# Performance work log

Hardware: AMD Instinct MI355X
Metric: run time of the kernel (lower is better)

## Reference

```python
import jax, jax.numpy as jnp
import numpy as np

B, D_IN, D_F = 4096, 1024, 256   # batch, extractor input dim, feature dim
M, K = 10, 8                      # n_mixtures, n_components per mixture
LOG2PI = float(np.log(2.0 * np.pi))


def setup_inputs() -> dict:
    key = jax.random.key(0)
    k0, k1, k2, k3, k4 = jax.random.split(key, 5)
    x = jax.random.normal(k0, (B, D_IN), jnp.float32)
    W = jax.random.normal(k1, (D_IN, D_F), jnp.float32) / np.sqrt(D_IN)
    b = jnp.zeros((D_F,), jnp.float32)
    means = jax.random.normal(k2, (M, K, D_F), jnp.float32)
    # full covariance parameter; tril is taken in forward; +I keeps the
    # Cholesky-factor diagonal positive, as torch MultivariateNormal requires
    covs = jax.random.normal(k3, (M, K, D_F, D_F), jnp.float32) * 0.01
    covs = covs + jnp.eye(D_F, dtype=jnp.float32)
    weights = jax.random.normal(k4, (M, K), jnp.float32)
    return {"x": x, "W": W, "b": b, "means": means, "covs": covs, "weights": weights}


def reference(x, W, b, means, covs, weights):
    # extractor: Linear + ReLU -> [B, D_F]
    feats = jax.nn.relu(x @ W + b)
    # scale_tril = tril(cov) for every (mixture, component): [M, K, D_F, D_F]
    L = jnp.tril(covs)
    # diff between every feature vector and every component mean: [M, K, B, D_F]
    diff = feats[None, None, :, :] - means[:, :, None, :]
    # batched triangular solve L z = diff^T -> z: [M, K, D_F, B]
    z = jax.scipy.linalg.solve_triangular(L, jnp.swapaxes(diff, -1, -2), lower=True)
    quad = jnp.sum(z * z, axis=-2)  # Mahalanobis term: [M, K, B]
    logdet = jnp.sum(jnp.log(jnp.diagonal(L, axis1=-2, axis2=-1)), axis=-1)  # [M, K]
    logp = -0.5 * (quad + D_F * LOG2PI) - logdet[..., None]  # MVN log_prob: [M, K, B]
    # per-mixture softmax over component weights, multiply into log-probs
    w = jax.nn.softmax(weights, axis=-1)  # [M, K]
    mix = w[..., None] * logp             # [M, K, B]
    # GMM returns [B, K]; DeepGMM stacks over mixtures and transposes -> [B, M, K]
    return jnp.transpose(mix, (2, 0, 1))
```

## Files before the change

### kernel.cpp

```cpp
#include <hip/hip_runtime.h>

#define B_N 4096
#define D_IN 1024
#define D_F 256
#define MK 80
#define LOG2PI 1.8378770664093453f
#define XP_S 72

typedef float f32x4 __attribute__((ext_vector_type(4)));
typedef short bf16x8 __attribute__((ext_vector_type(8)));
typedef float float4_ __attribute__((ext_vector_type(4)));
typedef unsigned int u32x4 __attribute__((ext_vector_type(4)));
typedef unsigned short u16x8 __attribute__((ext_vector_type(8)));

__device__ __forceinline__ unsigned short f2bf(float f) {
    unsigned u = __float_as_uint(f);
    u += 0x7fffu + ((u >> 16) & 1u);
    return (unsigned short)(u >> 16);
}
__device__ __forceinline__ float bf2f(unsigned short h) {
    return __uint_as_float(((unsigned)h) << 16);
}
__device__ __forceinline__ void gload_lds16(const void* g, void* l) {
    __builtin_amdgcn_global_load_lds((const __attribute__((address_space(1))) void*)g,
                                     (__attribute__((address_space(3))) void*)l, 16, 0, 0);
}
__device__ __forceinline__ bf16x8 pack8(float4_ a, float4_ b) {
    bf16x8 r;
    r[0] = (short)f2bf(a.x); r[1] = (short)f2bf(a.y);
    r[2] = (short)f2bf(a.z); r[3] = (short)f2bf(a.w);
    r[4] = (short)f2bf(b.x); r[5] = (short)f2bf(b.y);
    r[6] = (short)f2bf(b.z); r[7] = (short)f2bf(b.w);
    return r;
}

__global__ __launch_bounds__(256) void k_pre(const float* __restrict__ W,
                                             const float* __restrict__ covs,
                                             const float* __restrict__ wts,
                                             unsigned short* __restrict__ wt,
                                             float* __restrict__ wmix,
                                             float* __restrict__ ldet,
                                             unsigned short* __restrict__ covsb) {
    int bx = blockIdx.x, tid = threadIdx.x;
    if (bx < 64) {
        __shared__ unsigned short t[64][65];
        int k0 = (bx >> 2) * 64, n0 = (bx & 3) * 64;
        int r = tid / 64, c = tid % 64;
        #pragma unroll
        for (int rr = r; rr < 64; rr += 4)
            t[rr][c] = f2bf(W[(size_t)(k0 + rr) * D_F + n0 + c]);
        __syncthreads();
        #pragma unroll
        for (int rr = r; rr < 64; rr += 4)
            wt[(size_t)(n0 + rr) * D_IN + k0 + c] = t[c][rr];
    } else if (bx < 144) {
        if (tid < 64) {
            int mk = bx - 64;
            int l = tid;
            const float* Lm = covs + (size_t)mk * D_F * D_F;
            float s = 0.0f;
            for (int i = l; i < D_F; i += 64) s += logf(Lm[(size_t)i * D_F + i]);
            for (int off = 32; off; off >>= 1) s += __shfl_down(s, off);
            if (l == 0) {
                ldet[mk] = s;
                int m = mk / 8, k = mk % 8;
                float mx = -1e30f;
                for (int j = 0; j < 8; j++) mx = fmaxf(mx, wts[m * 8 + j]);
                float sum = 0.0f;
                for (int j = 0; j < 8; j++) sum += expf(wts[m * 8 + j] - mx);
                wmix[mk] = expf(wts[m * 8 + k] - mx) / sum;
            }
        }
    } else if (bx < 224) {
        int mk = bx - 144;
        const float* Cm = covs + (size_t)mk * D_F * D_F;
        unsigned short* Cb = covsb + (size_t)mk * 10 * 4096;
        #pragma unroll
        for (int I = 1; I < 4; ++I)
            for (int K = 0; K < I; ++K) {
                int idx = (I * (I - 1)) / 2 + K;
                for (int t4 = tid; t4 < 1024; t4 += 256) {
                    int r = t4 >> 4, kq = t4 & 15;
                    float4_ v = *(const float4_*)&Cm[(size_t)(I * 64 + r) * D_F
                                                     + K * 64 + kq * 4];
                    ushort4 o;
                    o.x = f2bf(v.x); o.y = f2bf(v.y); o.z = f2bf(v.z); o.w = f2bf(v.w);
                    *(ushort4*)&Cb[(size_t)idx * 4096 + r * 64 + kq * 4] = o;
                }
            }
    } else {
        int b = bx - 224;
        int mk = b >> 2, I = b & 3;
        int i0 = I * 64;
        __shared__ float rl[64];
        __shared__ unsigned short X[64][XP_S];
        __shared__ unsigned short Yt[2][64][XP_S];
        int w = tid >> 6, l = tid & 63;
        const float* Cm = covs + (size_t)mk * D_F * D_F;
        if (tid < 64) rl[tid] = 1.0f / Cm[(size_t)(i0 + tid) * D_F + i0 + tid];
        __syncthreads();
        for (int t4 = tid; t4 < 1024; t4 += 256) {
            int r = t4 >> 4, kq = t4 & 15;
            float4_ v = *(const float4_*)&Cm[(size_t)(i0 + r) * D_F + i0 + kq * 4];
            float ri = rl[r];
            int base = kq * 4;
            ushort4 o;
            o.x = (base     < r) ? f2bf(v.x * ri) : (unsigned short)0;
            o.y = (base + 1 < r) ? f2bf(v.y * ri) : (unsigned short)0;
            o.z = (base + 2 < r) ? f2bf(v.z * ri) : (unsigned short)0;
            o.w = (base + 3 < r) ? f2bf(v.w * ri) : (unsigned short)0;
            *(ushort4*)&X[r][base] = o;
        }
        __syncthreads();
        for (int t = tid; t < 4096; t += 256) {
            int j = t >> 6, i = t & 63;
            unsigned short xv = X[i][j];
            Yt[0][j][i] = (i == j) ? (unsigned short)0x3F80
                                   : (unsigned short)(xv ^ 0x8000u);
        }
        __syncthreads();
        int cur = 0;
        for (int it = 0; it < 3; ++it) {
            bf16x8 a0 = *(const bf16x8*)&Yt[cur][16 * w + (l & 15)][(l >> 4) * 8];
            bf16x8 a1 = *(const bf16x8*)&Yt[cur][16 * w + (l & 15)][32 + (l >> 4) * 8];
            f32x4 acc[4] = {{0, 0, 0, 0}, {0, 0, 0, 0}, {0, 0, 0, 0}, {0, 0, 0, 0}};
            #pragma unroll
            for (int ni = 0; ni < 4; ++ni) {
                bf16x8 b0 = *(const bf16x8*)&X[ni * 16 + (l & 15)][(l >> 4) * 8];
                bf16x8 b1 = *(const bf16x8*)&X[ni * 16 + (l & 15)][32 + (l >> 4) * 8];
                acc[ni] = __builtin_amdgcn_mfma_f32_16x16x32_bf16(a0, b0, acc[ni], 0, 0, 0);
                acc[ni] = __builtin_amdgcn_mfma_f32_16x16x32_bf16(a1, b1, acc[ni], 0, 0, 0);
            }
            #pragma unroll
            for (int ni = 0; ni < 4; ++ni)
                #pragma unroll
                for (int q = 0; q < 4; ++q) {
                    int i = ni * 16 + (l & 15);
                    int j = 16 * w + (l >> 4) * 4 + q;
                    float v = ((i == j) ? 1.0f : 0.0f) - acc[ni][q];
                    Yt[cur ^ 1][j][i] = f2bf(v);
                }
            __syncthreads();
            cur ^= 1;
        }
        unsigned short* Xg = covsb + ((size_t)mk * 10 + 6 + I) * 4096;
        for (int t = tid; t < 4096; t += 256) {
            int r = t >> 6, c = t & 63;
            Xg[t] = f2bf(bf2f(Yt[cur][c][r]) * rl[c]);
        }
    }
}

__global__ __launch_bounds__(256) void k_inv_panel(
        const unsigned short* __restrict__ covsb,
        const float* __restrict__ means,
        unsigned short* __restrict__ linv,
        float* __restrict__ cpart) {
    int mk = blockIdx.x, J = blockIdx.y;
    int jc0 = J * 64;
    __shared__ unsigned short Xp[4][64][XP_S];
    __shared__ unsigned short Sb[64][XP_S];
    __shared__ float muS[64];
    int tid = threadIdx.x, w = tid >> 6, l = tid & 63;
    const unsigned short* Cb = covsb + (size_t)mk * 10 * 4096;
    const unsigned short* Dmk = Cb + 6 * 4096;
    unsigned short* Lout = linv + (size_t)mk * D_F * D_F;

    for (int t = tid; t < jc0 * 8; t += 256) {
        int r = t >> 3, s = t & 7;
        ((u32x4*)(Lout + (size_t)r * D_F + jc0))[s] = (u32x4){0, 0, 0, 0};
    }
    const unsigned short* DJ = Dmk + J * 4096;
    for (int t = tid; t < 4096; t += 256) {
        int r = t >> 6, c = t & 63;
        Xp[J][c][r] = DJ[t];
    }
    for (int t = tid; t < 512; t += 256) {
        int r = t >> 3, s = t & 7;
        ((u32x4*)(Lout + (size_t)(jc0 + r) * D_F + jc0))[s] = ((const u32x4*)(DJ + r * 64))[s];
    }
    __syncthreads();

    for (int I = J + 1; I < 4; ++I) {
        f32x4 acc[4] = {};
        for (int K = J; K < I; ++K) {
            const unsigned short* CB = Cb + (size_t)((I * (I - 1)) / 2 + K) * 4096;
            #pragma unroll
            for (int kb = 0; kb < 2; ++kb) {
                bf16x8 af = *(const bf16x8*)&Xp[K][w * 16 + (l & 15)][kb * 32 + (l >> 4) * 8];
                #pragma unroll
                for (int ni = 0; ni < 4; ++ni) {
                    bf16x8 bf = *(const bf16x8*)&CB[(size_t)(ni * 16 + (l & 15)) * 64
                                                    + kb * 32 + (l >> 4) * 8];
                    acc[ni] = __builtin_amdgcn_mfma_f32_16x16x32_bf16(af, bf, acc[ni], 0, 0, 0);
                }
            }
        }
        #pragma unroll
        for (int ni = 0; ni < 4; ++ni)
            #pragma unroll
            for (int q = 0; q < 4; ++q)
                Sb[w * 16 + ((l >> 4) << 2) + q][ni * 16 + (l & 15)] = f2bf(acc[ni][q]);
        __syncthreads();
        f32x4 acc2[4] = {};
        #pragma unroll
        for (int kb = 0; kb < 2; ++kb) {
            bf16x8 af = *(const bf16x8*)&Sb[w * 16 + (l & 15)][kb * 32 + (l >> 4) * 8];
            #pragma unroll
            for (int ni = 0; ni < 4; ++ni) {
                const u16x8* dp = (const u16x8*)(Dmk + (size_t)I * 4096
                                  + (ni * 16 + (l & 15)) * 64 + kb * 32 + (l >> 4) * 8);
                u16x8 dv = *dp ^ (unsigned short)0x8000;
                bf16x8 bf = __builtin_bit_cast(bf16x8, dv);
                acc2[ni] = __builtin_amdgcn_mfma_f32_16x16x32_bf16(af, bf, acc2[ni], 0, 0, 0);
            }
        }
        #pragma unroll
        for (int ni = 0; ni < 4; ++ni)
            #pragma unroll
            for (int q = 0; q < 4; ++q) {
                int c = w * 16 + ((l >> 4) << 2) + q;
                int r = ni * 16 + (l & 15);
                unsigned short hv = f2bf(acc2[ni][q]);
                Xp[I][c][r] = hv;
                Lout[(size_t)(I * 64 + r) * D_F + jc0 + c] = hv;
            }
        __syncthreads();
    }

    if (tid < 64) muS[tid] = means[(size_t)mk * D_F + jc0 + tid];
    __syncthreads();
    {
        int I = w, r = l;
        float s = 0.0f;
        if (I >= J) {
            for (int c = 0; c < 64; ++c)
                s += bf2f(Xp[I][c][r]) * muS[c];
        }
        cpart[((size_t)mk * 4 + J) * 256 + tid] = s;
    }
}

__global__ __launch_bounds__(256) void k_feat(const float* __restrict__ x,
                                              const unsigned short* __restrict__ wt,
                                              const float* __restrict__ bias,
                                              unsigned short* __restrict__ fb) {
    __shared__ unsigned short As[64][128];
    __shared__ unsigned short Bs[64][128];
    int b0 = blockIdx.x * 64;
    int n0 = blockIdx.y * 64;
    int tid = threadIdx.x, w = tid >> 6, l = tid & 63;
    int wm = w >> 1, wn = w & 1;
    f32x4 acc[2][2] = {};
    for (int k0 = 0; k0 < D_IN; k0 += 128) {
        float4_ av[4][2];
        #pragma unroll
        for (int it = 0; it < 4; ++it) {
            int o16 = tid + it * 256;
            int r = o16 >> 4, c = o16 & 15;
            const float* gp = x + (size_t)(b0 + r) * D_IN + k0 + c * 8;
            av[it][0] = *(const float4_*)gp;
            av[it][1] = *(const float4_*)(gp + 4);
        }
        __syncthreads();
        #pragma unroll
        for (int it = 0; it < 4; ++it) {
            int o16 = tid + it * 256;
            int r = o16 >> 4, c = o16 & 15;
            int cs = c ^ (r & 7);
            *(bf16x8*)&As[r][cs * 8] = pack8(av[it][0], av[it][1]);
            gload_lds16(wt + (size_t)(n0 + r) * D_IN + k0 + cs * 8, &Bs[0][0] + o16 * 8);
        }
        __syncthreads();
        #pragma unroll
        for (int ks = 0; ks < 4; ++ks) {
            int uw = ((ks * 4 + (l >> 4)) ^ (l & 7)) * 8;
            bf16x8 af[2], bg[2];
            #pragma unroll
            for (int mi = 0; mi < 2; ++mi)
                af[mi] = *(const bf16x8*)&As[wm * 32 + mi * 16 + (l & 15)][uw];
            #pragma unroll
            for (int ni = 0; ni < 2; ++ni)
                bg[ni] = *(const bf16x8*)&Bs[wn * 32 + ni * 16 + (l & 15)][uw];
            #pragma unroll
            for (int mi = 0; mi < 2; ++mi)
                #pragma unroll
                for (int ni = 0; ni < 2; ++ni)
                    acc[mi][ni] = __builtin_amdgcn_mfma_f32_16x16x32_bf16(
                        af[mi], bg[ni], acc[mi][ni], 0, 0, 0);
        }
    }
    #pragma unroll
    for (int mi = 0; mi < 2; ++mi)
        #pragma unroll
        for (int ni = 0; ni < 2; ++ni) {
            int d = n0 + wn * 32 + ni * 16 + (l & 15);
            float bia = bias[d];
            #pragma unroll
            for (int r = 0; r < 4; ++r) {
                int b = b0 + wm * 32 + mi * 16 + (l >> 4) * 4 + r;
                float v = fmaxf(acc[mi][ni][r] + bia, 0.0f);
                fb[(size_t)b * D_F + d] = f2bf(v);
            }
        }
}

__global__ __launch_bounds__(512) void k_gmm(const unsigned short* __restrict__ linv,
                                             const unsigned short* __restrict__ fb,
                                             const float* __restrict__ cpart,
                                             const float* __restrict__ wmix,
                                             const float* __restrict__ ldet,
                                             float* __restrict__ out) {
    __shared__ unsigned short As[256][64];
    __shared__ unsigned short Bs[128][64];
    __shared__ float cb[D_F];
    __shared__ float qpart[4][128];
    int mk = blockIdx.x;
    int b0 = blockIdx.y * 128;
    int tid = threadIdx.x, w = tid >> 6, l = tid & 63;
    int wm = w >> 1, wn = w & 1;
    const unsigned short* Ab = linv + (size_t)mk * D_F * D_F;
    if (tid < D_F) {
        const float* cp = cpart + (size_t)mk * 4 * D_F + tid;
        cb[tid] = cp[0] + cp[256] + cp[512] + cp[768];
    }
    f32x4 acc[4][4] = {};
    for (int k0 = 0; k0 < D_F; k0 += 64) {
        #pragma unroll
        for (int it = 0; it < 4; ++it) {
            int o16 = tid + it * 512;
            int r = o16 >> 3, c8 = (o16 & 7) ^ (r & 7);
            gload_lds16(Ab + (size_t)r * D_F + k0 + c8 * 8, &As[0][0] + o16 * 8);
        }
        #pragma unroll
        for (int it = 0; it < 2; ++it) {
            int o16 = tid + it * 512;
            int r = o16 >> 3, c8 = (o16 & 7) ^ (r & 7);
            gload_lds16(fb + (size_t)(b0 + r) * D_F + k0 + c8 * 8, &Bs[0][0] + o16 * 8);
        }
        __syncthreads();
        #pragma unroll
        for (int ks = 0; ks < 2; ++ks) {
            int uw = ((ks * 4 + (l >> 4)) ^ (l & 7)) * 8;
            bf16x8 af[4], bg[4];
            #pragma unroll
            for (int mi = 0; mi < 4; ++mi)
                af[mi] = *(const bf16x8*)&As[wm * 64 + mi * 16 + (l & 15)][uw];
            #pragma unroll
            for (int ni = 0; ni < 4; ++ni)
                bg[ni] = *(const bf16x8*)&Bs[wn * 64 + ni * 16 + (l & 15)][uw];
            #pragma unroll
            for (int mi = 0; mi < 4; ++mi)
                #pragma unroll
                for (int ni = 0; ni < 4; ++ni)
                    acc[mi][ni] = __builtin_amdgcn_mfma_f32_16x16x32_bf16(
                        af[mi], bg[ni], acc[mi][ni], 0, 0, 0);
        }
        __syncthreads();
    }
    float p[4] = {0, 0, 0, 0};
    #pragma unroll
    for (int mi = 0; mi < 4; ++mi) {
        int ibase = wm * 64 + mi * 16 + ((l >> 4) << 2);
        #pragma unroll
        for (int r = 0; r < 4; ++r) {
            float cv = cb[ibase + r];
            #pragma unroll
            for (int ni = 0; ni < 4; ++ni) {
                float z = acc[mi][ni][r] - cv;
                p[ni] += z * z;
            }
        }
    }
    #pragma unroll
    for (int ni = 0; ni < 4; ++ni) {
        p[ni] += __shfl_xor(p[ni], 16);
        p[ni] += __shfl_xor(p[ni], 32);
    }
    if (l < 16) {
        #pragma unroll
        for (int ni = 0; ni < 4; ++ni)
            qpart[wm][wn * 64 + ni * 16 + l] = p[ni];
    }
    __syncthreads();
    if (tid < 128) {
        float q = qpart[0][tid] + qpart[1][tid] + qpart[2][tid] + qpart[3][tid];
        float lp = -0.5f * (q + (float)D_F * LOG2PI) - ldet[mk];
        out[(size_t)(b0 + tid) * MK + mk] = wmix[mk] * lp;
    }
}

extern "C" void kernel_launch(void* const* d_in, const int* in_sizes, int n_in,
                              void* d_out, int out_size, void* d_ws, size_t ws_size,
                              hipStream_t stream) {
    const float* x     = (const float*)d_in[0];
    const float* W     = (const float*)d_in[1];
    const float* bias  = (const float*)d_in[2];
    const float* means = (const float*)d_in[3];
    const float* covs  = (const float*)d_in[4];
    const float* wts   = (const float*)d_in[5];
    float* out = (float*)d_out;

    char* ws = (char*)d_ws;
    unsigned short* covsb = (unsigned short*)(ws);
    unsigned short* wt    = (unsigned short*)(ws + 6553600);
    unsigned short* fb    = (unsigned short*)(ws + 7077888);
    unsigned short* linv  = (unsigned short*)(ws + 9175040);
    float* wmix = (float*)(ws + 19742720);
    float* ldet = (float*)(ws + 19743040);
    float* cpart = (float*)(ws + 6553600);

    k_pre<<<dim3(544), dim3(256), 0, stream>>>(W, covs, wts, wt, wmix, ldet, covsb);
    k_feat<<<dim3(64, 4), dim3(256), 0, stream>>>(x, wt, bias, fb);
    k_inv_panel<<<dim3(MK, 4), dim3(256), 0, stream>>>(covsb, means, linv, cpart);
    k_gmm<<<dim3(MK, 32), dim3(512), 0, stream>>>(linv, fb, cpart, wmix, ldet, out);
}
```

Baseline: 82.90 us.

## Merge feature GEMM into preprocessing kernel, split W transpose into own launch

Moves the W transpose into a small standalone kernel and folds the feature GEMM into the former preprocessing kernel as extra blocks, so the GEMM runs alongside the log-det, covariance bf16 conversion and diagonal-block inverse work. Shared memory becomes one 32 KB buffer reused by each branch. The aim is to overlap independent stages and fill the GPU better instead of running them back to back. In exchange, every block of the merged kernel now reserves 32 KB of LDS, which can lower occupancy for the lighter branches.

```diff
diff --git a/kernel.cpp b/kernel.cpp
--- a/kernel.cpp
+++ b/kernel.cpp
@@ -34,28 +34,95 @@
     return r;
 }
 
-__global__ __launch_bounds__(256) void k_pre(const float* __restrict__ W,
+__global__ __launch_bounds__(256) void k_wt(const float* __restrict__ W,
+                                            unsigned short* __restrict__ wt) {
+    __shared__ unsigned short t[64][65];
+    int bx = blockIdx.x, tid = threadIdx.x;
+    int k0 = (bx >> 2) * 64, n0 = (bx & 3) * 64;
+    int r = tid / 64, c = tid % 64;
+    #pragma unroll
+    for (int rr = r; rr < 64; rr += 4)
+        t[rr][c] = f2bf(W[(size_t)(k0 + rr) * D_F + n0 + c]);
+    __syncthreads();
+    #pragma unroll
+    for (int rr = r; rr < 64; rr += 4)
+        wt[(size_t)(n0 + rr) * D_IN + k0 + c] = t[c][rr];
+}
+
+__global__ __launch_bounds__(256) void k_mid(const float* __restrict__ x,
+                                             const unsigned short* __restrict__ wt,
+                                             const float* __restrict__ bias,
                                              const float* __restrict__ covs,
                                              const float* __restrict__ wts,
-                                             unsigned short* __restrict__ wt,
+                                             unsigned short* __restrict__ fb,
                                              float* __restrict__ wmix,
                                              float* __restrict__ ldet,
                                              unsigned short* __restrict__ covsb) {
+    __shared__ char smem[32768];
     int bx = blockIdx.x, tid = threadIdx.x;
-    if (bx < 64) {
-        __shared__ unsigned short t[64][65];
-        int k0 = (bx >> 2) * 64, n0 = (bx & 3) * 64;
-        int r = tid / 64, c = tid % 64;
-        #pragma unroll
-        for (int rr = r; rr < 64; rr += 4)
-            t[rr][c] = f2bf(W[(size_t)(k0 + rr) * D_F + n0 + c]);
-        __syncthreads();
-        #pragma unroll
-        for (int rr = r; rr < 64; rr += 4)
-            wt[(size_t)(n0 + rr) * D_IN + k0 + c] = t[c][rr];
-    } else if (bx < 144) {
+    if (bx < 256) {
+        unsigned short(*As)[128] = (unsigned short(*)[128])smem;
+        unsigned short(*Bs)[128] = (unsigned short(*)[128])(smem + 16384);
+        int b0 = (bx >> 2) * 64;
+        int n0 = (bx & 3) * 64;
+        int w = tid >> 6, l = tid & 63;
+        int wm = w >> 1, wn = w & 1;
+        f32x4 acc[2][2] = {};
+        for (int k0 = 0; k0 < D_IN; k0 += 128) {
+            float4_ av[4][2];
+            #pragma unroll
+            for (int it = 0; it < 4; ++it) {
+                int o16 = tid + it * 256;
+                int r = o16 >> 4, c = o16 & 15;
+                const float* gp = x + (size_t)(b0 + r) * D_IN + k0 + c * 8;
+                av[it][0] = *(const float4_*)gp;
+                av[it][1] = *(const float4_*)(gp + 4);
+            }
+            __syncthreads();
+            #pragma unroll
+            for (int it = 0; it < 4; ++it) {
+                int o16 = tid + it * 256;
+                int r = o16 >> 4, c = o16 & 15;
+                int cs = c ^ (r & 7);
+                *(bf16x8*)&As[r][cs * 8] = pack8(av[it][0], av[it][1]);
+                gload_lds16(wt + (size_t)(n0 + r) * D_IN + k0 + cs * 8,
+                            &Bs[0][0] + o16 * 8);
+            }
+            __syncthreads();
+            #pragma unroll
+            for (int ks = 0; ks < 4; ++ks) {
+                int uw = ((ks * 4 + (l >> 4)) ^ (l & 7)) * 8;
+                bf16x8 af[2], bg[2];
+                #pragma unroll
+                for (int mi = 0; mi < 2; ++mi)
+                    af[mi] = *(const bf16x8*)&As[wm * 32 + mi * 16 + (l & 15)][uw];
+                #pragma unroll
+                for (int ni = 0; ni < 2; ++ni)
+                    bg[ni] = *(const bf16x8*)&Bs[wn * 32 + ni * 16 + (l & 15)][uw];
+                #pragma unroll
+                for (int mi = 0; mi < 2; ++mi)
+                    #pragma unroll
+                    for (int ni = 0; ni < 2; ++ni)
+                        acc[mi][ni] = __builtin_amdgcn_mfma_f32_16x16x32_bf16(
+                            af[mi], bg[ni], acc[mi][ni], 0, 0, 0);
+            }
+        }
+        #pragma unroll
+        for (int mi = 0; mi < 2; ++mi)
+            #pragma unroll
+            for (int ni = 0; ni < 2; ++ni) {
+                int d = n0 + wn * 32 + ni * 16 + (l & 15);
+                float bia = bias[d];
+                #pragma unroll
+                for (int r = 0; r < 4; ++r) {
+                    int b = b0 + wm * 32 + mi * 16 + (l >> 4) * 4 + r;
+                    float v = fmaxf(acc[mi][ni][r] + bia, 0.0f);
+                    fb[(size_t)b * D_F + d] = f2bf(v);
+                }
+            }
+    } else if (bx < 336) {
         if (tid < 64) {
-            int mk = bx - 64;
+            int mk = bx - 256;
             int l = tid;
             const float* Lm = covs + (size_t)mk * D_F * D_F;
             float s = 0.0f;
@@ -71,8 +138,8 @@
                 wmix[mk] = expf(wts[m * 8 + k] - mx) / sum;
             }
         }
-    } else if (bx < 224) {
-        int mk = bx - 144;
+    } else if (bx < 416) {
+        int mk = bx - 336;
         const float* Cm = covs + (size_t)mk * D_F * D_F;
         unsigned short* Cb = covsb + (size_t)mk * 10 * 4096;
         #pragma unroll
@@ -89,12 +156,12 @@
                 }
             }
     } else {
-        int b = bx - 224;
+        int b = bx - 416;
         int mk = b >> 2, I = b & 3;
         int i0 = I * 64;
-        __shared__ float rl[64];
-        __shared__ unsigned short X[64][XP_S];
-        __shared__ unsigned short Yt[2][64][XP_S];
+        float* rl = (float*)smem;
+        unsigned short(*X)[XP_S] = (unsigned short(*)[XP_S])(smem + 256);
+        unsigned short(*Yt)[64][XP_S] = (unsigned short(*)[64][XP_S])(smem + 9472);
         int w = tid >> 6, l = tid & 63;
         const float* Cm = covs + (size_t)mk * D_F * D_F;
         if (tid < 64) rl[tid] = 1.0f / Cm[(size_t)(i0 + tid) * D_F + i0 + tid];
@@ -239,70 +306,6 @@
         }
         cpart[((size_t)mk * 4 + J) * 256 + tid] = s;
     }
-}
-
-__global__ __launch_bounds__(256) void k_feat(const float* __restrict__ x,
-                                              const unsigned short* __restrict__ wt,
-                                              const float* __restrict__ bias,
-                                              unsigned short* __restrict__ fb) {
-    __shared__ unsigned short As[64][128];
-    __shared__ unsigned short Bs[64][128];
-    int b0 = blockIdx.x * 64;
-    int n0 = blockIdx.y * 64;
-    int tid = threadIdx.x, w = tid >> 6, l = tid & 63;
-    int wm = w >> 1, wn = w & 1;
-    f32x4 acc[2][2] = {};
-    for (int k0 = 0; k0 < D_IN; k0 += 128) {
-        float4_ av[4][2];
-        #pragma unroll
-        for (int it = 0; it < 4; ++it) {
-            int o16 = tid + it * 256;
-            int r = o16 >> 4, c = o16 & 15;
-            const float* gp = x + (size_t)(b0 + r) * D_IN + k0 + c * 8;
-            av[it][0] = *(const float4_*)gp;
-            av[it][1] = *(const float4_*)(gp + 4);
-        }
-        __syncthreads();
-        #pragma unroll
-        for (int it = 0; it < 4; ++it) {
-            int o16 = tid + it * 256;
-            int r = o16 >> 4, c = o16 & 15;
-            int cs = c ^ (r & 7);
-            *(bf16x8*)&As[r][cs * 8] = pack8(av[it][0], av[it][1]);
-            gload_lds16(wt + (size_t)(n0 + r) * D_IN + k0 + cs * 8, &Bs[0][0] + o16 * 8);
-        }
-        __syncthreads();
-        #pragma unroll
-        for (int ks = 0; ks < 4; ++ks) {
-            int uw = ((ks * 4 + (l >> 4)) ^ (l & 7)) * 8;
-            bf16x8 af[2], bg[2];
-            #pragma unroll
-            for (int mi = 0; mi < 2; ++mi)
-                af[mi] = *(const bf16x8*)&As[wm * 32 + mi * 16 + (l & 15)][uw];
-            #pragma unroll
-            for (int ni = 0; ni < 2; ++ni)
-                bg[ni] = *(const bf16x8*)&Bs[wn * 32 + ni * 16 + (l & 15)][uw];
-            #pragma unroll
-            for (int mi = 0; mi < 2; ++mi)
-                #pragma unroll
-                for (int ni = 0; ni < 2; ++ni)
-                    acc[mi][ni] = __builtin_amdgcn_mfma_f32_16x16x32_bf16(
-                        af[mi], bg[ni], acc[mi][ni], 0, 0, 0);
-        }
-    }
-    #pragma unroll
-    for (int mi = 0; mi < 2; ++mi)
-        #pragma unroll
-        for (int ni = 0; ni < 2; ++ni) {
-            int d = n0 + wn * 32 + ni * 16 + (l & 15);
-            float bia = bias[d];
-            #pragma unroll
-            for (int r = 0; r < 4; ++r) {
-                int b = b0 + wm * 32 + mi * 16 + (l >> 4) * 4 + r;
-                float v = fmaxf(acc[mi][ni][r] + bia, 0.0f);
-                fb[(size_t)b * D_F + d] = f2bf(v);
-            }
-        }
 }
 
 __global__ __launch_bounds__(512) void k_gmm(const unsigned short* __restrict__ linv,
@@ -410,8 +413,9 @@
     float* ldet = (float*)(ws + 19743040);
     float* cpart = (float*)(ws + 6553600);
 
-    k_pre<<<dim3(544), dim3(256), 0, stream>>>(W, covs, wts, wt, wmix, ldet, covsb);
-    k_feat<<<dim3(64, 4), dim3(256), 0, stream>>>(x, wt, bias, fb);
+    k_wt<<<dim3(64), dim3(256), 0, stream>>>(W, wt);
+    k_mid<<<dim3(736), dim3(256), 0, stream>>>(x, wt, bias, covs, wts,
+                                               fb, wmix, ldet, covsb);
     k_inv_panel<<<dim3(MK, 4), dim3(256), 0, stream>>>(covsb, means, linv, cpart);
     k_gmm<<<dim3(MK, 32), dim3(512), 0, stream>>>(linv, fb, cpart, wmix, ldet, out);
 }
```

New measurement: 88.31 us. +6.5%, slower.
